# Performance work log

Hardware: AMD Instinct MI355X
Metric: run time of the kernel (lower is better)

The kernel has to match this reference:

```python
import jax, jax.numpy as jnp
import numpy as np

N_NODES = 50000
N_EDGES = 600000
IN_CH = 128
HID_CH = 128
OUT_CH = 64
DEMO = 8
N_GRAPHS = 100


def setup_inputs() -> dict:
    key = jax.random.key(0)
    ks = jax.random.split(key, 16)
    s = 0.02
    inp = {
        "x": jax.random.normal(ks[0], (N_NODES, IN_CH), jnp.float32),
        "edge_index": jax.random.randint(ks[1], (2, N_EDGES), 0, N_NODES, jnp.int32),
        "batch": jnp.sort(jax.random.randint(ks[2], (N_NODES,), 0, N_GRAPHS, jnp.int32)),
        "demographic": jax.random.normal(ks[3], (N_GRAPHS, DEMO), jnp.float32),
        "W1": jax.random.normal(ks[4], (IN_CH, HID_CH), jnp.float32) * s,
        "b1": jnp.zeros((HID_CH,), jnp.float32),
        "W2": jax.random.normal(ks[5], (HID_CH, HID_CH), jnp.float32) * s,
        "b2": jnp.zeros((HID_CH,), jnp.float32),
        "W3": jax.random.normal(ks[6], (HID_CH, OUT_CH), jnp.float32) * s,
        "b3": jnp.zeros((OUT_CH,), jnp.float32),
        "Wf1": jax.random.normal(ks[7], (OUT_CH + DEMO, 64), jnp.float32) * s,
        "bf1": jnp.zeros((64,), jnp.float32),
        "Wf2": jax.random.normal(ks[8], (64, 32), jnp.float32) * s,
        "bf2": jnp.zeros((32,), jnp.float32),
        "Wf3": jax.random.normal(ks[9], (32, 2), jnp.float32) * s,
        "bf3": jnp.zeros((2,), jnp.float32),
    }
    return inp


def _gcn_conv(x, W, b, src, dst, norm, n_nodes):
    # PyG GCNConv: out_i = sum_j norm_ij * (x_j @ W) + b  (self-loops included in src/dst)
    h = x @ W
    msg = h[src] * norm[:, None]
    return jax.ops.segment_sum(msg, dst, num_segments=n_nodes) + b


def reference(x, edge_index, batch, demographic, W1, b1, W2, b2, W3, b3, Wf1, bf1, Wf2, bf2, Wf3, bf3):
    n = x.shape[0]
    # add self-loops
    loop = jnp.arange(n, dtype=edge_index.dtype)
    src = jnp.concatenate([edge_index[0], loop])
    dst = jnp.concatenate([edge_index[1], loop])
    # symmetric degree normalization: deg^{-1/2}[src] * deg^{-1/2}[dst]
    deg = jax.ops.segment_sum(jnp.ones_like(src, jnp.float32), dst, num_segments=n)
    dinv = jnp.where(deg > 0, jax.lax.rsqrt(deg), 0.0)
    norm = dinv[src] * dinv[dst]

    h = jax.nn.relu(_gcn_conv(x, W1, b1, src, dst, norm, n))
    h = jax.nn.relu(_gcn_conv(h, W2, b2, src, dst, norm, n))
    h = jax.nn.relu(_gcn_conv(h, W3, b3, src, dst, norm, n))

    # global mean pool over graphs
    g = demographic.shape[0]
    sums = jax.ops.segment_sum(h, batch, num_segments=g)
    cnts = jax.ops.segment_sum(jnp.ones((n,), jnp.float32), batch, num_segments=g)
    pooled = sums / jnp.maximum(cnts, 1.0)[:, None]

    z = jnp.concatenate([pooled, demographic], axis=1)
    z = jax.nn.relu(z @ Wf1 + bf1)
    z = jax.nn.relu(z @ Wf2 + bf2)
    return z @ Wf3 + bf3
```

## Files before the change

### kernel.cpp

```cpp
#include <hip/hip_runtime.h>


typedef __bf16 bf16x8 __attribute__((ext_vector_type(8)));
typedef float f32x4 __attribute__((ext_vector_type(4)));
typedef float f32x2 __attribute__((ext_vector_type(2)));

__device__ __forceinline__ unsigned char f32_to_fp8(float v) {
    return (unsigned char)(__builtin_amdgcn_cvt_pk_fp8_f32(v, 0.f, 0, false) & 0xff);
}
__device__ __forceinline__ void acc8_fp8(float* a, uint2 u) {
    f32x2 v;
    v = __builtin_amdgcn_cvt_pk_f32_fp8(u.x, false); a[0] += v.x; a[1] += v.y;
    v = __builtin_amdgcn_cvt_pk_f32_fp8(u.x, true);  a[2] += v.x; a[3] += v.y;
    v = __builtin_amdgcn_cvt_pk_f32_fp8(u.y, false); a[4] += v.x; a[5] += v.y;
    v = __builtin_amdgcn_cvt_pk_f32_fp8(u.y, true);  a[6] += v.x; a[7] += v.y;
}

union BF2 {
    __bf16 h[2];
    unsigned u;
};

#define PAD(c) (((c) + 7) & ~7)
#define BCAP 64
#define ECHUNK 4096
#define ECAP 4096
#define BUCKCAP 4096

__device__ __forceinline__ void wpack_block(const float* __restrict__ W,
                                            __bf16* __restrict__ hi,
                                            __bf16* __restrict__ lo, int N, int b, int l) {
    int t = b >> 2, c = b & 3;
    int k0 = c * 32 + (l >> 4) * 8;
    int ncol = t * 16 + (l & 15);
    size_t base = ((size_t)b * 64 + l) * 8;
#pragma unroll
    for (int j = 0; j < 8; j++) {
        float v = W[(size_t)(k0 + j) * N + ncol];
        __bf16 h = (__bf16)v;
        hi[base + j] = h;
        lo[base + j] = (__bf16)(v - (float)h);
    }
}

__global__ __launch_bounds__(1024) void k_bin(const int* __restrict__ src,
                                              const int* __restrict__ dst,
                                              int2* __restrict__ binbuf,
                                              int* __restrict__ bcnt,
                                              const int* __restrict__ batch,
                                              int* __restrict__ gstart,
                                              const float* __restrict__ W1,
                                              const float* __restrict__ W2,
                                              const float* __restrict__ W3,
                                              __bf16* __restrict__ Wp1h, __bf16* __restrict__ Wp1l,
                                              __bf16* __restrict__ Wp2h, __bf16* __restrict__ Wp2l,
                                              __bf16* __restrict__ Wp3h, __bf16* __restrict__ Wp3l,
                                              int E, int EC, int nbuck, int n, int G) {
    int b = blockIdx.x;
    int tid = threadIdx.x;
    if (b < EC) {
        __shared__ int lcur[512];
        for (int i = tid; i < nbuck; i += 1024) lcur[i] = 0;
        __syncthreads();
        int e0 = b * ECHUNK;
        int cntE = E - e0;
        if (cntE > ECHUNK) cntE = ECHUNK;
#pragma unroll
        for (int k = 0; k < 4; k++) {
            int idx = tid + k * 1024;
            if (idx < cntE) {
                int s = src[e0 + idx];
                int d = dst[e0 + idx];
                int bk = d >> 7;
                int slot = atomicAdd(&lcur[bk], 1);
                if (slot < BCAP) {
                    int2 sd = {s, d};
                    binbuf[((size_t)b * nbuck + bk) * BCAP + slot] = sd;
                }
            }
        }
        __syncthreads();
        for (int bk = tid; bk < nbuck; bk += 1024) {
            int c = lcur[bk];
            bcnt[b * nbuck + bk] = (c < BCAP) ? c : BCAP;
        }
        return;
    }
    if (b == EC) {
        int g = tid;
        if (g <= G) {
            int lo = 0, hi = n;
            while (lo < hi) {
                int mid = (lo + hi) >> 1;
                if (batch[mid] < g) lo = mid + 1; else hi = mid;
            }
            gstart[g] = lo;
        }
        return;
    }
    int b64 = (b - EC - 1) * 16 + (tid >> 6);
    int l = tid & 63;
    if (b64 < 32) wpack_block(W1, Wp1h, Wp1l, 128, b64, l);
    else if (b64 < 64) wpack_block(W2, Wp2h, Wp2l, 128, b64 - 32, l);
    else if (b64 < 80) wpack_block(W3, Wp3h, Wp3l, 64, b64 - 64, l);
}

__global__ __launch_bounds__(1024) void k_csr(const int2* __restrict__ binbuf,
                                              const int* __restrict__ bcnt,
                                              float* __restrict__ dinv,
                                              int2* __restrict__ rowspan,
                                              int* __restrict__ col,
                                              unsigned int* __restrict__ tz128,
                                              unsigned int* __restrict__ tz64,
                                              int n, int EC, int nbuck) {
    __shared__ int lcnt[160];
    __shared__ int lpre[161];
    __shared__ int deg[128];
    __shared__ int lloc[129];
    __shared__ int lfill[128];
    __shared__ int sedge[ECAP];
    __shared__ unsigned char redge[ECAP];
    __shared__ int cols_s[BUCKCAP];
    int b = blockIdx.x;
    int tid = threadIdx.x;
    int lane = tid & 63;
    int wid = tid >> 6;
    int r0 = b << 7;
    int r1 = r0 + 128;
    if (r1 > n) r1 = n;
    int nrows = r1 - r0;
    if (b == 0) {
        if (tid < 32) tz128[(size_t)n * 32 + tid] = 0u;
        else if (tid < 48) tz64[(size_t)n * 16 + (tid - 32)] = 0u;
    }
    for (int c = tid; c < EC; c += 1024) lcnt[c] = bcnt[c * nbuck + b];
    if (tid < 128) deg[tid] = 0;
    __syncthreads();
    if (wid == 0) {
        int carry = 0;
        for (int bb = 0; bb < EC; bb += 64) {
            int idx = bb + lane;
            int val = (idx < EC) ? lcnt[idx] : 0;
            int sc = val;
#pragma unroll
            for (int d = 1; d < 64; d <<= 1) {
                int o = __shfl_up(sc, d);
                if (lane >= d) sc += o;
            }
            int grp = __shfl(sc, 63);
            if (idx < EC) lpre[idx] = sc - val + carry;
            carry += grp;
        }
        if (lane == 0) lpre[EC] = carry;
    }
    __syncthreads();
    int T = lpre[EC];
    for (int i = tid; i < T; i += 1024) {
        int lo = 0, hi = EC;
        while (lo < hi) {
            int mid = (lo + hi) >> 1;
            if (lpre[mid + 1] <= i) lo = mid + 1; else hi = mid;
        }
        int j = i - lpre[lo];
        int2 sd = binbuf[((size_t)lo * nbuck + b) * BCAP + j];
        unsigned r = (unsigned)(sd.y - r0);
        bool ok = r < (unsigned)nrows;
        if (ok) atomicAdd(&deg[r], 1);
        if (i < ECAP) {
            sedge[i] = sd.x;
            redge[i] = ok ? (unsigned char)r : (unsigned char)255;
        }
    }
    __syncthreads();
    if (wid == 0) {
        int carry = 0;
#pragma unroll
        for (int bb = 0; bb < 128; bb += 64) {
            int idx = bb + lane;
            int val = (idx < nrows) ? PAD(deg[idx]) : 0;
            int sc = val;
#pragma unroll
            for (int d = 1; d < 64; d <<= 1) {
                int o = __shfl_up(sc, d);
                if (lane >= d) sc += o;
            }
            int grp = __shfl(sc, 63);
            lloc[idx] = sc - val + carry;
            carry += grp;
        }
        if (lane == 0) lloc[128] = carry;
    }
    __syncthreads();
    int base = b * BUCKCAP;
    int tot = lloc[128];
    if (tot > BUCKCAP) tot = BUCKCAP;
    if (tid < nrows) {
        int d = deg[tid];
        lfill[tid] = lloc[tid];
        dinv[r0 + tid] = rsqrtf((float)(d + 1));
        int st = base + lloc[tid];
        int2 sp = {st, st + d};
        rowspan[r0 + tid] = sp;
    }
    for (int i = tid; i < tot; i += 1024) cols_s[i] = n;
    __syncthreads();
    int Tc = (T < ECAP) ? T : ECAP;
    for (int i = tid; i < Tc; i += 1024) {
        int r = redge[i];
        if (r != 255) {
            int pos = atomicAdd(&lfill[r], 1);
            if (pos < BUCKCAP) cols_s[pos] = sedge[i];
        }
    }
    for (int i = ECAP + tid; i < T; i += 1024) {
        int lo = 0, hi = EC;
        while (lo < hi) {
            int mid = (lo + hi) >> 1;
            if (lpre[mid + 1] <= i) lo = mid + 1; else hi = mid;
        }
        int j = i - lpre[lo];
        int2 sd = binbuf[((size_t)lo * nbuck + b) * BCAP + j];
        unsigned r = (unsigned)(sd.y - r0);
        if (r < (unsigned)nrows) {
            int pos = atomicAdd(&lfill[r], 1);
            if (pos < BUCKCAP) cols_s[pos] = sd.x;
        }
    }
    __syncthreads();
    for (int i = tid; i < tot; i += 1024) col[base + i] = cols_s[i];
}

__global__ __launch_bounds__(256) void k_gemm1(const float* __restrict__ A,
                                               const __bf16* __restrict__ Wp_hi,
                                               const __bf16* __restrict__ Wp_lo,
                                               const float* __restrict__ dinv,
                                               unsigned char* __restrict__ Cf8, int n) {
    constexpr int NT = 8;
    constexpr int N = NT * 16;
    int wave = (int)((blockIdx.x * 256u + threadIdx.x) >> 6);
    int lane = threadIdx.x & 63;
    int row0 = wave * 16;
    if (row0 >= n) return;
    int m = lane & 15;
    int q = lane >> 4;
    int row = row0 + m;
    if (row >= n) row = n - 1;
    const float* ap = A + (size_t)row * 128 + q * 8;
    bf16x8 ahi[4], alo[4];
#pragma unroll
    for (int c = 0; c < 4; c++) {
        float4 v0 = *(const float4*)(ap + c * 32);
        float4 v1 = *(const float4*)(ap + c * 32 + 4);
        float vv[8] = {v0.x, v0.y, v0.z, v0.w, v1.x, v1.y, v1.z, v1.w};
#pragma unroll
        for (int j = 0; j < 8; j++) {
            __bf16 h = (__bf16)vv[j];
            ahi[c][j] = h;
            alo[c][j] = (__bf16)(vv[j] - (float)h);
        }
    }
    float dscale[4];
#pragma unroll
    for (int r = 0; r < 4; r++) {
        int rr = row0 + q * 4 + r;
        dscale[r] = dinv[rr < n ? rr : (n - 1)];
    }
#pragma unroll
    for (int t = 0; t < NT; t++) {
        f32x4 acc = {0.f, 0.f, 0.f, 0.f};
#pragma unroll
        for (int c = 0; c < 4; c++) {
            size_t off = ((size_t)(t * 4 + c) * 64 + lane) * 8;
            bf16x8 bh = *(const bf16x8*)(Wp_hi + off);
            bf16x8 bl = *(const bf16x8*)(Wp_lo + off);
            acc = __builtin_amdgcn_mfma_f32_16x16x32_bf16(ahi[c], bh, acc, 0, 0, 0);
            acc = __builtin_amdgcn_mfma_f32_16x16x32_bf16(alo[c], bh, acc, 0, 0, 0);
            acc = __builtin_amdgcn_mfma_f32_16x16x32_bf16(ahi[c], bl, acc, 0, 0, 0);
        }
        int colx = t * 16 + m;
#pragma unroll
        for (int r = 0; r < 4; r++) {
            int orow = row0 + q * 4 + r;
            if (orow < n) Cf8[(size_t)orow * N + colx] = f32_to_fp8(acc[r] * dscale[r]);
        }
    }
}

template <int NT>
__global__ __launch_bounds__(256) void k_gemm_bf16(const __bf16* __restrict__ A,
                                                   const __bf16* __restrict__ Wp_hi,
                                                   const __bf16* __restrict__ Wp_lo,
                                                   const float* __restrict__ dinv,
                                                   unsigned char* __restrict__ Cf8, int n) {
    constexpr int N = NT * 16;
    int wave = (int)((blockIdx.x * 256u + threadIdx.x) >> 6);
    int lane = threadIdx.x & 63;
    int row0 = wave * 16;
    if (row0 >= n) return;
    int m = lane & 15;
    int q = lane >> 4;
    int row = row0 + m;
    if (row >= n) row = n - 1;
    const __bf16* ap = A + (size_t)row * 128 + q * 8;
    bf16x8 a[4];
#pragma unroll
    for (int c = 0; c < 4; c++) a[c] = *(const bf16x8*)(ap + c * 32);
    float dscale[4];
#pragma unroll
    for (int r = 0; r < 4; r++) {
        int rr = row0 + q * 4 + r;
        dscale[r] = dinv[rr < n ? rr : (n - 1)];
    }
#pragma unroll
    for (int t = 0; t < NT; t++) {
        f32x4 acc = {0.f, 0.f, 0.f, 0.f};
#pragma unroll
        for (int c = 0; c < 4; c++) {
            size_t off = ((size_t)(t * 4 + c) * 64 + lane) * 8;
            bf16x8 bh = *(const bf16x8*)(Wp_hi + off);
            bf16x8 bl = *(const bf16x8*)(Wp_lo + off);
            acc = __builtin_amdgcn_mfma_f32_16x16x32_bf16(a[c], bh, acc, 0, 0, 0);
            acc = __builtin_amdgcn_mfma_f32_16x16x32_bf16(a[c], bl, acc, 0, 0, 0);
        }
        int colx = t * 16 + m;
#pragma unroll
        for (int r = 0; r < 4; r++) {
            int orow = row0 + q * 4 + r;
            if (orow < n) Cf8[(size_t)orow * N + colx] = f32_to_fp8(acc[r] * dscale[r]);
        }
    }
}

__global__ __launch_bounds__(256) void k_agg128(const unsigned char* __restrict__ t8,
                                                const int2* __restrict__ rowspan,
                                                const int* __restrict__ col,
                                                const float* __restrict__ dinv,
                                                const float* __restrict__ bias,
                                                unsigned int* __restrict__ out, int n) {
    int w = (int)((blockIdx.x * 256u + threadIdx.x) >> 6);
    int lane = threadIdx.x & 63;
    if (w >= n) return;
    const uint2* t8v = (const uint2*)t8;
    int cg = lane & 15;
    int g = lane >> 4;
    float acc[8] = {0.f, 0.f, 0.f, 0.f, 0.f, 0.f, 0.f, 0.f};
    int2 rs = rowspan[w];
    int p = rs.x, pe = rs.y;
    for (; p < pe; p += 8) {
        int c0 = col[p + g];
        int c1 = col[p + 4 + g];
        uint2 u0 = t8v[((size_t)c0 << 4) + cg];
        uint2 u1 = t8v[((size_t)c1 << 4) + cg];
        acc8_fp8(acc, u0);
        acc8_fp8(acc, u1);
    }
#pragma unroll
    for (int j = 0; j < 8; j++) {
        acc[j] += __shfl_xor(acc[j], 16);
        acc[j] += __shfl_xor(acc[j], 32);
    }
    {
        uint2 us = t8v[((size_t)w << 4) + cg];
        float s8[8] = {0.f, 0.f, 0.f, 0.f, 0.f, 0.f, 0.f, 0.f};
        acc8_fp8(s8, us);
#pragma unroll
        for (int j = 0; j < 8; j++) acc[j] += s8[j];
    }
    float di = dinv[w];
    float4 bb0 = *(const float4*)(bias + cg * 8);
    float4 bb1 = *(const float4*)(bias + cg * 8 + 4);
    float bv[8] = {bb0.x, bb0.y, bb0.z, bb0.w, bb1.x, bb1.y, bb1.z, bb1.w};
    BF2 o[4];
#pragma unroll
    for (int j = 0; j < 4; j++) {
        o[j].h[0] = (__bf16)fmaxf(di * acc[2 * j] + bv[2 * j], 0.f);
        o[j].h[1] = (__bf16)fmaxf(di * acc[2 * j + 1] + bv[2 * j + 1], 0.f);
    }
    if (lane < 16) {
        uint4 st = {o[0].u, o[1].u, o[2].u, o[3].u};
        *(uint4*)(out + (size_t)w * 64 + cg * 4) = st;
    }
}

__global__ __launch_bounds__(256) void k_agg64(const unsigned char* __restrict__ t8,
                                               const int2* __restrict__ rowspan,
                                               const int* __restrict__ col,
                                               const float* __restrict__ dinv,
                                               const float* __restrict__ bias,
                                               __bf16* __restrict__ out, int n) {
    int w = (int)((blockIdx.x * 256u + threadIdx.x) >> 6);
    int lane = threadIdx.x & 63;
    if (w >= n) return;
    const uint2* t8v = (const uint2*)t8;
    int cg = lane & 7;
    int g = lane >> 3;
    float acc[8] = {0.f, 0.f, 0.f, 0.f, 0.f, 0.f, 0.f, 0.f};
    int2 rs = rowspan[w];
    int p = rs.x, pe = rs.y;
    for (; p < pe; p += 8) {
        int c = col[p + g];
        uint2 u = t8v[((size_t)c << 3) + cg];
        acc8_fp8(acc, u);
    }
#pragma unroll
    for (int j = 0; j < 8; j++) {
        acc[j] += __shfl_xor(acc[j], 8);
        acc[j] += __shfl_xor(acc[j], 16);
        acc[j] += __shfl_xor(acc[j], 32);
    }
    {
        uint2 us = t8v[((size_t)w << 3) + cg];
        float s8[8] = {0.f, 0.f, 0.f, 0.f, 0.f, 0.f, 0.f, 0.f};
        acc8_fp8(s8, us);
#pragma unroll
        for (int j = 0; j < 8; j++) acc[j] += s8[j];
    }
    float di = dinv[w];
    float4 bb0 = *(const float4*)(bias + cg * 8);
    float4 bb1 = *(const float4*)(bias + cg * 8 + 4);
    float bv[8] = {bb0.x, bb0.y, bb0.z, bb0.w, bb1.x, bb1.y, bb1.z, bb1.w};
    BF2 o[4];
#pragma unroll
    for (int j = 0; j < 4; j++) {
        o[j].h[0] = (__bf16)fmaxf(di * acc[2 * j] + bv[2 * j], 0.f);
        o[j].h[1] = (__bf16)fmaxf(di * acc[2 * j + 1] + bv[2 * j + 1], 0.f);
    }
    if (lane < 8) {
        uint4 st = {o[0].u, o[1].u, o[2].u, o[3].u};
        *(uint4*)((unsigned int*)out + (size_t)w * 32 + cg * 4) = st;
    }
}

__global__ __launch_bounds__(256) void k_poolmlp(const unsigned short* __restrict__ h,
                                                 const int* __restrict__ gstart,
                                                 const float* __restrict__ demo,
                                                 const float* __restrict__ Wf1,
                                                 const float* __restrict__ bf1,
                                                 const float* __restrict__ Wf2,
                                                 const float* __restrict__ bf2,
                                                 const float* __restrict__ Wf3,
                                                 const float* __restrict__ bf3,
                                                 float* __restrict__ out, int G) {
    int g = blockIdx.x;
    int tid = threadIdx.x;
    int lane = tid & 63;
    int wv = tid >> 6;
    int s = gstart[g], e = gstart[g + 1];
    const unsigned* hu = (const unsigned*)h;
    int cg = lane & 15;
    int sub = lane >> 4;
    float acc[4] = {0.f, 0.f, 0.f, 0.f};
    for (int i = s + wv * 4 + sub; i < e; i += 16) {
        uint2 v = *(const uint2*)(hu + ((size_t)i << 5) + cg * 2);
        acc[0] += __uint_as_float(v.x << 16);
        acc[1] += __uint_as_float(v.x & 0xffff0000u);
        acc[2] += __uint_as_float(v.y << 16);
        acc[3] += __uint_as_float(v.y & 0xffff0000u);
    }
#pragma unroll
    for (int j = 0; j < 4; j++) {
        acc[j] += __shfl_xor(acc[j], 16);
        acc[j] += __shfl_xor(acc[j], 32);
    }
    __shared__ float red[4][64];
    __shared__ float zin[72];
    __shared__ float z1[64];
    __shared__ float z2[32];
    if (sub == 0) {
#pragma unroll
        for (int j = 0; j < 4; j++) red[wv][cg * 4 + j] = acc[j];
    }
    if (tid >= 64 && tid < 72) zin[tid] = demo[g * 8 + (tid - 64)];
    __syncthreads();
    if (tid < 64) {
        float v = red[0][tid] + red[1][tid] + red[2][tid] + red[3][tid];
        zin[tid] = v / fmaxf((float)(e - s), 1.0f);
    }
    __syncthreads();
    if (tid < 64) {
        float a = bf1[tid];
        for (int k = 0; k < 72; k++) a += zin[k] * Wf1[k * 64 + tid];
        z1[tid] = fmaxf(a, 0.f);
    }
    __syncthreads();
    if (tid < 32) {
        float a2 = bf2[tid];
        for (int k = 0; k < 64; k++) a2 += z1[k] * Wf2[k * 32 + tid];
        z2[tid] = fmaxf(a2, 0.f);
    }
    __syncthreads();
    if (tid < 2) {
        float a3 = bf3[tid];
        for (int k = 0; k < 32; k++) a3 += z2[k] * Wf3[k * 2 + tid];
        out[g * 2 + tid] = a3;
    }
}

extern "C" void kernel_launch(void* const* d_in, const int* in_sizes, int n_in,
                              void* d_out, int out_size, void* d_ws, size_t ws_size,
                              hipStream_t stream) {
    const float* x    = (const float*)d_in[0];
    const int*   ei   = (const int*)d_in[1];
    const int*   batch= (const int*)d_in[2];
    const float* demo = (const float*)d_in[3];
    const float* W1   = (const float*)d_in[4];
    const float* b1   = (const float*)d_in[5];
    const float* W2   = (const float*)d_in[6];
    const float* b2   = (const float*)d_in[7];
    const float* W3   = (const float*)d_in[8];
    const float* b3   = (const float*)d_in[9];
    const float* Wf1  = (const float*)d_in[10];
    const float* bf1  = (const float*)d_in[11];
    const float* Wf2  = (const float*)d_in[12];
    const float* bf2  = (const float*)d_in[13];
    const float* Wf3  = (const float*)d_in[14];
    const float* bf3  = (const float*)d_in[15];
    float* out = (float*)d_out;

    const int n = in_sizes[0] / 128;
    const int E = in_sizes[1] / 2;
    const int G = in_sizes[3] / 8;
    const int EC = (E + ECHUNK - 1) / ECHUNK;
    const int nbuck = (n + 127) / 128;

    char* ws = (char*)d_ws;
    auto alloc = [&](size_t bytes) {
        char* p = ws;
        ws += (bytes + 255) & ~(size_t)255;
        return p;
    };
    float*  dinv    = (float*)alloc((size_t)n * 4);
    int2*   rowspan = (int2*)alloc((size_t)n * 8);
    int*    col     = (int*)alloc((size_t)nbuck * BUCKCAP * 4);
    int2*   binbuf  = (int2*)alloc((size_t)EC * nbuck * BCAP * 8);
    int*    bcnt    = (int*)alloc((size_t)EC * nbuck * 4);
    unsigned char* tbf  = (unsigned char*)alloc((size_t)(n + 1) * 128);
    __bf16* hbuf    = (__bf16*)alloc((size_t)n * 128 * 2);
    unsigned char* t3bf = (unsigned char*)alloc((size_t)(n + 1) * 64);
    __bf16* h3      = (__bf16*)alloc((size_t)n * 64 * 2);
    __bf16* Wp1h    = (__bf16*)alloc(128 * 128 * 2);
    __bf16* Wp1l    = (__bf16*)alloc(128 * 128 * 2);
    __bf16* Wp2h    = (__bf16*)alloc(128 * 128 * 2);
    __bf16* Wp2l    = (__bf16*)alloc(128 * 128 * 2);
    __bf16* Wp3h    = (__bf16*)alloc(128 * 64 * 2);
    __bf16* Wp3l    = (__bf16*)alloc(128 * 64 * 2);
    int*    gstart  = (int*)alloc((size_t)(G + 1) * 4);

    const int* srcv = ei;
    const int* dstv = ei + E;

    int waves = (n + 15) / 16;
    int gemm_blocks = (waves + 3) / 4;
    int agg_blocks = (int)(((size_t)n * 64 + 255) / 256);

    k_bin<<<EC + 1 + 5, 1024, 0, stream>>>(srcv, dstv, binbuf, bcnt, batch, gstart,
                                           W1, W2, W3, Wp1h, Wp1l, Wp2h, Wp2l,
                                           Wp3h, Wp3l, E, EC, nbuck, n, G);
    k_csr<<<nbuck, 1024, 0, stream>>>(binbuf, bcnt, dinv, rowspan, col,
                                      (unsigned int*)tbf, (unsigned int*)t3bf,
                                      n, EC, nbuck);
    k_gemm1<<<gemm_blocks, 256, 0, stream>>>(x, Wp1h, Wp1l, dinv, tbf, n);
    k_agg128<<<agg_blocks, 256, 0, stream>>>(tbf, rowspan, col,
                                             dinv, b1, (unsigned int*)hbuf, n);
    k_gemm_bf16<8><<<gemm_blocks, 256, 0, stream>>>(hbuf, Wp2h, Wp2l, dinv, tbf, n);
    k_agg128<<<agg_blocks, 256, 0, stream>>>(tbf, rowspan, col,
                                             dinv, b2, (unsigned int*)hbuf, n);
    k_gemm_bf16<4><<<gemm_blocks, 256, 0, stream>>>(hbuf, Wp3h, Wp3l, dinv, t3bf, n);
    k_agg64<<<agg_blocks, 256, 0, stream>>>(t3bf, rowspan, col,
                                            dinv, b3, h3, n);

    k_poolmlp<<<G, 256, 0, stream>>>((const unsigned short*)h3, gstart, demo,
                                     Wf1, bf1, Wf2, bf2, Wf3, bf3, out, G);
}
```

Before: 227.9 us.

## Build CSR with global atomic degree count and scatter fused into first GEMM

Replaces the two-pass bin-then-bucket CSR construction with a global atomic degree histogram, a per-bucket wave scan that sets row spans, dinv and fill pointers, and an atomic scatter of source columns. The scatter runs in the same launch as the first GEMM, so edge placement overlaps with the dense work. Rows are no longer padded to multiples of 8, so the aggregation kernels now bound-check column reads. This removes the large binbuf traffic and the binary searches, at the cost of global atomics with contention on popular destinations, an extra memset and kernel launch, and a non-deterministic column order.

```diff
diff --git a/kernel.cpp b/kernel.cpp
--- a/kernel.cpp
+++ b/kernel.cpp
@@ -21,10 +21,6 @@
     unsigned u;
 };
 
-#define PAD(c) (((c) + 7) & ~7)
-#define BCAP 64
-#define ECHUNK 4096
-#define ECAP 4096
 #define BUCKCAP 4096
 
 __device__ __forceinline__ void wpack_block(const float* __restrict__ W,
@@ -43,52 +39,62 @@
     }
 }
 
-__global__ __launch_bounds__(1024) void k_bin(const int* __restrict__ src,
-                                              const int* __restrict__ dst,
-                                              int2* __restrict__ binbuf,
-                                              int* __restrict__ bcnt,
-                                              const int* __restrict__ batch,
-                                              int* __restrict__ gstart,
-                                              const float* __restrict__ W1,
-                                              const float* __restrict__ W2,
-                                              const float* __restrict__ W3,
-                                              __bf16* __restrict__ Wp1h, __bf16* __restrict__ Wp1l,
-                                              __bf16* __restrict__ Wp2h, __bf16* __restrict__ Wp2l,
-                                              __bf16* __restrict__ Wp3h, __bf16* __restrict__ Wp3l,
-                                              int E, int EC, int nbuck, int n, int G) {
+__global__ __launch_bounds__(256) void k_deg(const int* __restrict__ dst,
+                                             int* __restrict__ gdeg, int E) {
+    int i = (int)(blockIdx.x * 256u + threadIdx.x);
+    if (i < E) atomicAdd(&gdeg[dst[i]], 1);
+}
+
+__global__ __launch_bounds__(64) void k_span(const int* __restrict__ gdeg,
+                                             float* __restrict__ dinv,
+                                             int2* __restrict__ rowspan,
+                                             int* __restrict__ fill,
+                                             const int* __restrict__ batch,
+                                             int* __restrict__ gstart,
+                                             const float* __restrict__ W1,
+                                             const float* __restrict__ W2,
+                                             const float* __restrict__ W3,
+                                             __bf16* __restrict__ Wp1h, __bf16* __restrict__ Wp1l,
+                                             __bf16* __restrict__ Wp2h, __bf16* __restrict__ Wp2l,
+                                             __bf16* __restrict__ Wp3h, __bf16* __restrict__ Wp3l,
+                                             unsigned int* __restrict__ tz128,
+                                             unsigned int* __restrict__ tz64,
+                                             int n, int nbuck, int G) {
     int b = blockIdx.x;
-    int tid = threadIdx.x;
-    if (b < EC) {
-        __shared__ int lcur[512];
-        for (int i = tid; i < nbuck; i += 1024) lcur[i] = 0;
-        __syncthreads();
-        int e0 = b * ECHUNK;
-        int cntE = E - e0;
-        if (cntE > ECHUNK) cntE = ECHUNK;
-#pragma unroll
-        for (int k = 0; k < 4; k++) {
-            int idx = tid + k * 1024;
-            if (idx < cntE) {
-                int s = src[e0 + idx];
-                int d = dst[e0 + idx];
-                int bk = d >> 7;
-                int slot = atomicAdd(&lcur[bk], 1);
-                if (slot < BCAP) {
-                    int2 sd = {s, d};
-                    binbuf[((size_t)b * nbuck + bk) * BCAP + slot] = sd;
-                }
+    int lane = threadIdx.x;
+    if (b < nbuck) {
+        int r0 = b << 7;
+        int nrows = n - r0;
+        if (nrows > 128) nrows = 128;
+        int base = b * BUCKCAP;
+        if (b == 0) {
+            if (lane < 32) tz128[(size_t)n * 32 + lane] = 0u;
+            else if (lane < 48) tz64[(size_t)n * 16 + (lane - 32)] = 0u;
+        }
+        int carry = 0;
+#pragma unroll
+        for (int half = 0; half < 2; half++) {
+            int idx = half * 64 + lane;
+            int d = (idx < nrows) ? gdeg[r0 + idx] : 0;
+            int sc = d;
+#pragma unroll
+            for (int s = 1; s < 64; s <<= 1) {
+                int o = __shfl_up(sc, s);
+                if (lane >= s) sc += o;
             }
-        }
-        __syncthreads();
-        for (int bk = tid; bk < nbuck; bk += 1024) {
-            int c = lcur[bk];
-            bcnt[b * nbuck + bk] = (c < BCAP) ? c : BCAP;
+            if (idx < nrows) {
+                int st = base + carry + sc - d;
+                int2 sp = {st, st + d};
+                rowspan[r0 + idx] = sp;
+                fill[r0 + idx] = st;
+                dinv[r0 + idx] = rsqrtf((float)(d + 1));
+            }
+            carry += __shfl(sc, 63);
         }
         return;
     }
-    if (b == EC) {
-        int g = tid;
-        if (g <= G) {
+    if (b == nbuck) {
+        for (int g = lane; g <= G; g += 64) {
             int lo = 0, hi = n;
             while (lo < hi) {
                 int mid = (lo + hi) >> 1;
@@ -98,147 +104,36 @@
         }
         return;
     }
-    int b64 = (b - EC - 1) * 16 + (tid >> 6);
-    int l = tid & 63;
-    if (b64 < 32) wpack_block(W1, Wp1h, Wp1l, 128, b64, l);
-    else if (b64 < 64) wpack_block(W2, Wp2h, Wp2l, 128, b64 - 32, l);
-    else if (b64 < 80) wpack_block(W3, Wp3h, Wp3l, 64, b64 - 64, l);
-}
-
-__global__ __launch_bounds__(1024) void k_csr(const int2* __restrict__ binbuf,
-                                              const int* __restrict__ bcnt,
-                                              float* __restrict__ dinv,
-                                              int2* __restrict__ rowspan,
-                                              int* __restrict__ col,
-                                              unsigned int* __restrict__ tz128,
-                                              unsigned int* __restrict__ tz64,
-                                              int n, int EC, int nbuck) {
-    __shared__ int lcnt[160];
-    __shared__ int lpre[161];
-    __shared__ int deg[128];
-    __shared__ int lloc[129];
-    __shared__ int lfill[128];
-    __shared__ int sedge[ECAP];
-    __shared__ unsigned char redge[ECAP];
-    __shared__ int cols_s[BUCKCAP];
+    int b64 = b - nbuck - 1;
+    if (b64 < 32) wpack_block(W1, Wp1h, Wp1l, 128, b64, lane);
+    else if (b64 < 64) wpack_block(W2, Wp2h, Wp2l, 128, b64 - 32, lane);
+    else if (b64 < 80) wpack_block(W3, Wp3h, Wp3l, 64, b64 - 64, lane);
+}
+
+__global__ __launch_bounds__(256) void k_pg1(const int* __restrict__ src,
+                                             const int* __restrict__ dst,
+                                             int* __restrict__ fill,
+                                             int* __restrict__ col,
+                                             int E, int PBLK,
+                                             const float* __restrict__ A,
+                                             const __bf16* __restrict__ Wp_hi,
+                                             const __bf16* __restrict__ Wp_lo,
+                                             const float* __restrict__ dinv,
+                                             unsigned char* __restrict__ Cf8, int n) {
     int b = blockIdx.x;
     int tid = threadIdx.x;
-    int lane = tid & 63;
-    int wid = tid >> 6;
-    int r0 = b << 7;
-    int r1 = r0 + 128;
-    if (r1 > n) r1 = n;
-    int nrows = r1 - r0;
-    if (b == 0) {
-        if (tid < 32) tz128[(size_t)n * 32 + tid] = 0u;
-        else if (tid < 48) tz64[(size_t)n * 16 + (tid - 32)] = 0u;
-    }
-    for (int c = tid; c < EC; c += 1024) lcnt[c] = bcnt[c * nbuck + b];
-    if (tid < 128) deg[tid] = 0;
-    __syncthreads();
-    if (wid == 0) {
-        int carry = 0;
-        for (int bb = 0; bb < EC; bb += 64) {
-            int idx = bb + lane;
-            int val = (idx < EC) ? lcnt[idx] : 0;
-            int sc = val;
-#pragma unroll
-            for (int d = 1; d < 64; d <<= 1) {
-                int o = __shfl_up(sc, d);
-                if (lane >= d) sc += o;
-            }
-            int grp = __shfl(sc, 63);
-            if (idx < EC) lpre[idx] = sc - val + carry;
-            carry += grp;
-        }
-        if (lane == 0) lpre[EC] = carry;
-    }
-    __syncthreads();
-    int T = lpre[EC];
-    for (int i = tid; i < T; i += 1024) {
-        int lo = 0, hi = EC;
-        while (lo < hi) {
-            int mid = (lo + hi) >> 1;
-            if (lpre[mid + 1] <= i) lo = mid + 1; else hi = mid;
-        }
-        int j = i - lpre[lo];
-        int2 sd = binbuf[((size_t)lo * nbuck + b) * BCAP + j];
-        unsigned r = (unsigned)(sd.y - r0);
-        bool ok = r < (unsigned)nrows;
-        if (ok) atomicAdd(&deg[r], 1);
-        if (i < ECAP) {
-            sedge[i] = sd.x;
-            redge[i] = ok ? (unsigned char)r : (unsigned char)255;
-        }
-    }
-    __syncthreads();
-    if (wid == 0) {
-        int carry = 0;
-#pragma unroll
-        for (int bb = 0; bb < 128; bb += 64) {
-            int idx = bb + lane;
-            int val = (idx < nrows) ? PAD(deg[idx]) : 0;
-            int sc = val;
-#pragma unroll
-            for (int d = 1; d < 64; d <<= 1) {
-                int o = __shfl_up(sc, d);
-                if (lane >= d) sc += o;
-            }
-            int grp = __shfl(sc, 63);
-            lloc[idx] = sc - val + carry;
-            carry += grp;
-        }
-        if (lane == 0) lloc[128] = carry;
-    }
-    __syncthreads();
-    int base = b * BUCKCAP;
-    int tot = lloc[128];
-    if (tot > BUCKCAP) tot = BUCKCAP;
-    if (tid < nrows) {
-        int d = deg[tid];
-        lfill[tid] = lloc[tid];
-        dinv[r0 + tid] = rsqrtf((float)(d + 1));
-        int st = base + lloc[tid];
-        int2 sp = {st, st + d};
-        rowspan[r0 + tid] = sp;
-    }
-    for (int i = tid; i < tot; i += 1024) cols_s[i] = n;
-    __syncthreads();
-    int Tc = (T < ECAP) ? T : ECAP;
-    for (int i = tid; i < Tc; i += 1024) {
-        int r = redge[i];
-        if (r != 255) {
-            int pos = atomicAdd(&lfill[r], 1);
-            if (pos < BUCKCAP) cols_s[pos] = sedge[i];
-        }
-    }
-    for (int i = ECAP + tid; i < T; i += 1024) {
-        int lo = 0, hi = EC;
-        while (lo < hi) {
-            int mid = (lo + hi) >> 1;
-            if (lpre[mid + 1] <= i) lo = mid + 1; else hi = mid;
-        }
-        int j = i - lpre[lo];
-        int2 sd = binbuf[((size_t)lo * nbuck + b) * BCAP + j];
-        unsigned r = (unsigned)(sd.y - r0);
-        if (r < (unsigned)nrows) {
-            int pos = atomicAdd(&lfill[r], 1);
-            if (pos < BUCKCAP) cols_s[pos] = sd.x;
-        }
-    }
-    __syncthreads();
-    for (int i = tid; i < tot; i += 1024) col[base + i] = cols_s[i];
-}
-
-__global__ __launch_bounds__(256) void k_gemm1(const float* __restrict__ A,
-                                               const __bf16* __restrict__ Wp_hi,
-                                               const __bf16* __restrict__ Wp_lo,
-                                               const float* __restrict__ dinv,
-                                               unsigned char* __restrict__ Cf8, int n) {
+    if (b < PBLK) {
+        int i = b * 256 + tid;
+        if (i < E) {
+            int pos = atomicAdd(&fill[dst[i]], 1);
+            col[pos] = src[i];
+        }
+        return;
+    }
     constexpr int NT = 8;
     constexpr int N = NT * 16;
-    int wave = (int)((blockIdx.x * 256u + threadIdx.x) >> 6);
-    int lane = threadIdx.x & 63;
+    int wave = (b - PBLK) * 4 + (tid >> 6);
+    int lane = tid & 63;
     int row0 = wave * 16;
     if (row0 >= n) return;
     int m = lane & 15;
@@ -347,8 +242,10 @@
     int2 rs = rowspan[w];
     int p = rs.x, pe = rs.y;
     for (; p < pe; p += 8) {
-        int c0 = col[p + g];
-        int c1 = col[p + 4 + g];
+        int i0 = p + g;
+        int i1 = p + 4 + g;
+        int c0 = (i0 < pe) ? col[i0] : n;
+        int c1 = (i1 < pe) ? col[i1] : n;
         uint2 u0 = t8v[((size_t)c0 << 4) + cg];
         uint2 u1 = t8v[((size_t)c1 << 4) + cg];
         acc8_fp8(acc, u0);
@@ -398,7 +295,8 @@
     int2 rs = rowspan[w];
     int p = rs.x, pe = rs.y;
     for (; p < pe; p += 8) {
-        int c = col[p + g];
+        int i0 = p + g;
+        int c = (i0 < pe) ? col[i0] : n;
         uint2 u = t8v[((size_t)c << 3) + cg];
         acc8_fp8(acc, u);
     }
@@ -520,7 +418,6 @@
     const int n = in_sizes[0] / 128;
     const int E = in_sizes[1] / 2;
     const int G = in_sizes[3] / 8;
-    const int EC = (E + ECHUNK - 1) / ECHUNK;
     const int nbuck = (n + 127) / 128;
 
     char* ws = (char*)d_ws;
@@ -531,9 +428,9 @@
     };
     float*  dinv    = (float*)alloc((size_t)n * 4);
     int2*   rowspan = (int2*)alloc((size_t)n * 8);
-    int*    col     = (int*)alloc((size_t)nbuck * BUCKCAP * 4);
-    int2*   binbuf  = (int2*)alloc((size_t)EC * nbuck * BCAP * 8);
-    int*    bcnt    = (int*)alloc((size_t)EC * nbuck * 4);
+    int*    gdeg    = (int*)alloc((size_t)n * 4);
+    int*    fill    = (int*)alloc((size_t)n * 4);
+    int*    col     = (int*)alloc((size_t)nbuck * BUCKCAP * 4 + 65536);
     unsigned char* tbf  = (unsigned char*)alloc((size_t)(n + 1) * 128);
     __bf16* hbuf    = (__bf16*)alloc((size_t)n * 128 * 2);
     unsigned char* t3bf = (unsigned char*)alloc((size_t)(n + 1) * 64);
@@ -552,14 +449,16 @@
     int waves = (n + 15) / 16;
     int gemm_blocks = (waves + 3) / 4;
     int agg_blocks = (int)(((size_t)n * 64 + 255) / 256);
-
-    k_bin<<<EC + 1 + 5, 1024, 0, stream>>>(srcv, dstv, binbuf, bcnt, batch, gstart,
-                                           W1, W2, W3, Wp1h, Wp1l, Wp2h, Wp2l,
-                                           Wp3h, Wp3l, E, EC, nbuck, n, G);
-    k_csr<<<nbuck, 1024, 0, stream>>>(binbuf, bcnt, dinv, rowspan, col,
-                                      (unsigned int*)tbf, (unsigned int*)t3bf,
-                                      n, EC, nbuck);
-    k_gemm1<<<gemm_blocks, 256, 0, stream>>>(x, Wp1h, Wp1l, dinv, tbf, n);
+    int PBLK = (E + 255) / 256;
+
+    hipMemsetAsync(gdeg, 0, (size_t)n * 4, stream);
+    k_deg<<<PBLK, 256, 0, stream>>>(dstv, gdeg, E);
+    k_span<<<nbuck + 1 + 80, 64, 0, stream>>>(gdeg, dinv, rowspan, fill, batch, gstart,
+                                              W1, W2, W3, Wp1h, Wp1l, Wp2h, Wp2l,
+                                              Wp3h, Wp3l, (unsigned int*)tbf,
+                                              (unsigned int*)t3bf, n, nbuck, G);
+    k_pg1<<<PBLK + gemm_blocks, 256, 0, stream>>>(srcv, dstv, fill, col, E, PBLK,
+                                                  x, Wp1h, Wp1l, dinv, tbf, n);
     k_agg128<<<agg_blocks, 256, 0, stream>>>(tbf, rowspan, col,
                                              dinv, b1, (unsigned int*)hbuf, n);
     k_gemm_bf16<8><<<gemm_blocks, 256, 0, stream>>>(hbuf, Wp2h, Wp2l, dinv, tbf, n);
```

Result: slower. 287.9 us (+26.3%).
